# Optimization experiments

Hardware: AMD Instinct MI355X
Metric: run time of the kernel (lower is better)

The kernel has to match this reference:

```python
import jax, jax.numpy as jnp
import numpy as np

C = 256          # channels
K = 7            # kernel_size
GC = 16          # group_channels (hardcoded in module)
G = C // GC      # groups = 16
RED = 4          # reduction_ratio
PAD = (K - 1) // 2
EPS = 1e-5


def _bn(x, gamma, beta, mean, var):
    # inference-mode BatchNorm2d over channel dim (axis=1)
    inv = gamma / jnp.sqrt(var + EPS)
    return x * inv[None, :, None, None] + (beta - mean * inv)[None, :, None, None]


def setup_inputs() -> dict:
    key = jax.random.key(0)
    ks = jax.random.split(key, 8)
    cm = C // RED  # 64
    x = jax.random.normal(ks[0], (4, C, 64, 64), dtype=jnp.float32)
    w1 = jax.random.normal(ks[1], (cm, C), dtype=jnp.float32) * (1.0 / np.sqrt(C))
    bn1_gamma = jnp.abs(jax.random.normal(ks[2], (cm,), dtype=jnp.float32)) + 0.5
    bn1_beta = jax.random.normal(ks[3], (cm,), dtype=jnp.float32) * 0.1
    bn1_mean = jnp.zeros((cm,), jnp.float32)
    bn1_var = jnp.ones((cm,), jnp.float32)
    w2 = jax.random.normal(ks[4], (K * K * G, cm), dtype=jnp.float32) * (1.0 / np.sqrt(cm))
    b2 = jax.random.normal(ks[5], (K * K * G,), dtype=jnp.float32) * 0.1
    bn2_gamma = jnp.abs(jax.random.normal(ks[6], (C,), dtype=jnp.float32)) + 0.5
    bn2_beta = jax.random.normal(ks[7], (C,), dtype=jnp.float32) * 0.1
    bn2_mean = jnp.zeros((C,), jnp.float32)
    bn2_var = jnp.ones((C,), jnp.float32)
    return {"x": x, "w1": w1, "bn1_gamma": bn1_gamma, "bn1_beta": bn1_beta,
            "bn1_mean": bn1_mean, "bn1_var": bn1_var, "w2": w2, "b2": b2,
            "bn2_gamma": bn2_gamma, "bn2_beta": bn2_beta,
            "bn2_mean": bn2_mean, "bn2_var": bn2_var}


def reference(x, w1, bn1_gamma, bn1_beta, bn1_mean, bn1_var,
              w2, b2, bn2_gamma, bn2_beta, bn2_mean, bn2_var):
    b, c, h, w = x.shape
    # weight branch: 1x1 conv (no bias) -> BN -> ReLU -> 1x1 conv (bias)
    t = jnp.einsum('oc,bchw->bohw', w1, x)
    t = jax.nn.relu(_bn(t, bn1_gamma, bn1_beta, bn1_mean, bn1_var))
    wgt = jnp.einsum('oc,bchw->bohw', w2, t) + b2[None, :, None, None]
    wgt = wgt.reshape(b, G, K * K, h, w)  # per-pixel kernel per group
    # unfold x: extract KxK patches (stride 1, pad PAD), torch ordering:
    # channel slowest, kernel row, kernel col fastest
    x_pad = jnp.pad(x, ((0, 0), (0, 0), (PAD, PAD), (PAD, PAD)))
    patches = jnp.stack([x_pad[:, :, i:i + h, j:j + w]
                         for i in range(K) for j in range(K)], axis=2)  # (b,c,K2,h,w)
    patches = patches.reshape(b, G, GC, K * K, h, w)
    out = jnp.einsum('bgckhw,bgkhw->bgchw', patches, wgt).reshape(b, c, h, w)
    return jax.nn.relu(_bn(out, bn2_gamma, bn2_beta, bn2_mean, bn2_var))
```

## Files before the change

kernel.cpp:

```cpp
#include <hip/hip_runtime.h>

#define BN 4
#define C 256
#define H 64
#define W 64
#define CM 64
#define G 16
#define GC 16
#define KS 7
#define K2 49
#define PADD 3
#define EPSV 1e-5f

#define TS 16
#define HALO_R 22
#define HROWF 32
#define HSLOTP 712

#define W1T_OFF 0
#define B2P_OFF (W1T_OFF + C*CM)
#define S1_OFF  (B2P_OFF + G*64)
#define B1_OFF  (S1_OFF + CM)
#define S2_OFF  (B1_OFF + CM)
#define B2C_OFF (S2_OFF + C)
#define ZERO_OFF (B2C_OFF + C)
#define ABF_OFF (ZERO_OFF + 16)
#define TBF_OFF (ABF_OFF + 32768)

typedef __attribute__((ext_vector_type(8))) short bf16x8;
typedef __attribute__((ext_vector_type(4))) float f32x4;

__device__ __forceinline__ uint f2bf_rne(float f) {
  uint u = __float_as_uint(f);
  return (u + 0x7fffu + ((u >> 16) & 1u)) >> 16;
}

__device__ __forceinline__ void gload_lds4(const float* g, float* l) {
  __builtin_amdgcn_global_load_lds(
      (const __attribute__((address_space(1))) void*)g,
      (__attribute__((address_space(3))) void*)l, 4, 0, 0);
}

#define WAITBAR(N) do {                                            \
    asm volatile("s_waitcnt vmcnt(" #N ") lgkmcnt(0)" ::: "memory"); \
    __builtin_amdgcn_s_barrier();                                  \
    __builtin_amdgcn_sched_barrier(0);                             \
  } while (0)

#define BARRIER_ONLY() do {                                        \
    asm volatile("s_waitcnt lgkmcnt(0)" ::: "memory");             \
    __builtin_amdgcn_s_barrier();                                  \
    __builtin_amdgcn_sched_barrier(0);                             \
  } while (0)

__global__ __launch_bounds__(256) void prep_kernel(
    const float* __restrict__ w1, const float* __restrict__ w2,
    const float* __restrict__ b2,
    const float* __restrict__ g1, const float* __restrict__ be1,
    const float* __restrict__ m1, const float* __restrict__ v1,
    const float* __restrict__ g2, const float* __restrict__ be2,
    const float* __restrict__ m2, const float* __restrict__ v2,
    float* __restrict__ ws) {
  int tid = blockIdx.x * 256 + threadIdx.x;
  int nthr = gridDim.x * 256;
  for (int i = tid; i < CM * C; i += nthr) {
    int o = i / C, c = i - o * C;
    ws[W1T_OFF + c * CM + o] = w1[i];
  }
  {
    ushort* abf = (ushort*)(ws + ABF_OFF);
    for (int i = tid; i < G * 4 * 2 * 64 * 8; i += nthr) {
      int j = i & 7, lane = (i >> 3) & 63, ks = (i >> 9) & 1;
      int mt = (i >> 10) & 3, g = (i >> 12) & 15;
      int m = mt * 16 + (lane & 15);
      int o = ks * 32 + ((lane >> 4) << 3) + j;
      float v = (m < K2) ? w2[(g * K2 + m) * CM + o] : 0.f;
      abf[i] = (ushort)f2bf_rne(v);
    }
  }
  for (int i = tid; i < G * 64; i += nthr) {
    int g = i >> 6, k = i & 63;
    ws[B2P_OFF + i] = (k < K2) ? b2[g * K2 + k] : 0.f;
  }
  if (tid < CM) {
    float inv = g1[tid] * rsqrtf(v1[tid] + EPSV);
    ws[S1_OFF + tid] = inv;
    ws[B1_OFF + tid] = be1[tid] - m1[tid] * inv;
  }
  if (tid < C) {
    float inv = g2[tid] * rsqrtf(v2[tid] + EPSV);
    ws[S2_OFF + tid] = inv;
    ws[B2C_OFF + tid] = be2[tid] - m2[tid] * inv;
  }
  if (tid < 16) ws[ZERO_OFF + tid] = 0.f;
}

__global__ __launch_bounds__(256) void t_kernel(
    const float* __restrict__ x, float* __restrict__ ws) {
  __shared__ float part[4][32][64];
  int p = threadIdx.x & 63;
  int q = __builtin_amdgcn_readfirstlane(threadIdx.x >> 6);
  int y = blockIdx.x, b = blockIdx.y, oh = blockIdx.z;
  const float* __restrict__ w1T = ws + W1T_OFF + oh * 32;

  float acc[32];
#pragma unroll
  for (int o = 0; o < 32; ++o) acc[o] = 0.f;
  const float* __restrict__ xrow = x + (((size_t)b * C + q * 64) * H + y) * W;
#pragma unroll 2
  for (int cc = 0; cc < 64; ++cc) {
    float xv = xrow[(size_t)cc * H * W + p];
    const float* __restrict__ wr = w1T + (q * 64 + cc) * CM;
#pragma unroll
    for (int o = 0; o < 32; ++o) acc[o] = fmaf(wr[o], xv, acc[o]);
  }
#pragma unroll
  for (int o = 0; o < 32; ++o) part[q][o][p] = acc[o];
  __syncthreads();

  int tile = (y >> 4) * 4 + (p >> 4);
  int pix = (y & 15) * 16 + (p & 15);
  const float* __restrict__ s1 = ws + S1_OFF + oh * 32;
  const float* __restrict__ b1 = ws + B1_OFF + oh * 32;
  float fv[8];
#pragma unroll
  for (int i = 0; i < 8; ++i) {
    int o = q * 8 + i;
    float s = part[0][o][p] + part[1][o][p] + part[2][o][p] + part[3][o][p];
    fv[i] = fmaxf(fmaf(s, s1[o], b1[o]), 0.f);
  }
  uint4 pk;
  pk.x = f2bf_rne(fv[0]) | (f2bf_rne(fv[1]) << 16);
  pk.y = f2bf_rne(fv[2]) | (f2bf_rne(fv[3]) << 16);
  pk.z = f2bf_rne(fv[4]) | (f2bf_rne(fv[5]) << 16);
  pk.w = f2bf_rne(fv[6]) | (f2bf_rne(fv[7]) << 16);
  ushort* tbf = (ushort*)(ws + TBF_OFF);
  size_t idx = (((size_t)(b * 16 + tile) * 256 + pix) * 64) + oh * 32 + q * 8;
  *(uint4*)(tbf + idx) = pk;
}

__global__ __launch_bounds__(256, 3) void inv_kernel(
    const float* __restrict__ x, const float* __restrict__ ws,
    float* __restrict__ out) {
  __shared__ uint wgt_u[25][256];
  __shared__ float xh[2][4][HSLOTP];

  int tid = threadIdx.x;
  int lane = tid & 63;
  int wv = __builtin_amdgcn_readfirstlane(tid >> 6);
  int c16 = lane & 15, q = lane >> 4;
  int py = tid >> 4, chl = (tid >> 2) & 3, pq = tid & 3;
  int px0 = pq << 2;
  int tile = blockIdx.x, g = blockIdx.y, b = blockIdx.z;
  int ty = (tile >> 2) * TS, tx = (tile & 3) * TS;

  const ushort* abf = (const ushort*)(ws + ABF_OFF);
  const ushort* tbf = (const ushort*)(ws + TBF_OFF);

  float scv[4], bcv[4];
#pragma unroll
  for (int p = 0; p < 4; ++p) {
    scv[p] = ws[S2_OFF + g * GC + p * 4 + chl];
    bcv[p] = ws[B2C_OFF + g * GC + p * 4 + chl];
  }

  bf16x8 afr[4][2], bfr[4][2];
  f32x4 bias[4];
#pragma unroll
  for (int mt = 0; mt < 4; ++mt) {
#pragma unroll
    for (int ks = 0; ks < 2; ++ks)
      afr[mt][ks] = *(const bf16x8*)(abf + ((g * 8 + mt * 2 + ks) * 64 + lane) * 8);
    bias[mt] = *(const f32x4*)(ws + B2P_OFF + g * 64 + mt * 16 + q * 4);
  }
#pragma unroll
  for (int nt = 0; nt < 4; ++nt) {
    int pix = wv * 64 + nt * 16 + c16;
#pragma unroll
    for (int ks = 0; ks < 2; ++ks)
      bfr[nt][ks] = *(const bf16x8*)(
          tbf + (((size_t)(b * 16 + tile) * 256 + pix) * 64 + ks * 32 + q * 8));
  }

  uint hmask = 0;
  int hofs[11];
#pragma unroll
  for (int t2 = 0; t2 < 11; ++t2) {
    int f = t2 * 64 + lane;
    int row = f >> 5, cp = (f >> 2) & 7, sub = f & 3;
    int s8 = (row + 3 * (row >> 3)) & 7;
    int col = ((cp ^ s8) << 2) + sub;
    int gy = ty + row - PADD, gx = tx + col - PADD;
    bool v = (col < HALO_R) && ((unsigned)gy < H) && ((unsigned)gx < W);
    hmask |= (uint)v << t2;
    hofs[t2] = gy * W + gx;
  }
  const float* zsrc = ws + ZERO_OFF;
  const float* xg = x + ((size_t)b * C + g * GC) * (H * W);

#define STAGE(CH, BUF) do {                                         \
    const float* xc_ = xg + (size_t)(CH) * (H * W);                 \
    float* dst_ = &xh[BUF][(CH) & 3][0];                            \
    _Pragma("unroll")                                               \
    for (int t2 = 0; t2 < 11; ++t2) {                               \
      const float* s_ = ((hmask >> t2) & 1u) ? (xc_ + hofs[t2]) : zsrc; \
      gload_lds4(s_, dst_ + t2 * 64);                               \
    }                                                               \
  } while (0)

  STAGE(wv, 0);
  STAGE(4 + wv, 1);

#pragma unroll
  for (int nt = 0; nt < 4; ++nt) {
    f32x4 a[4];
#pragma unroll
    for (int mt = 0; mt < 4; ++mt) a[mt] = bias[mt];
#pragma unroll
    for (int ks = 0; ks < 2; ++ks)
#pragma unroll
      for (int mt = 0; mt < 4; ++mt)
        a[mt] = __builtin_amdgcn_mfma_f32_16x16x32_bf16(afr[mt][ks], bfr[nt][ks],
                                                        a[mt], 0, 0, 0);
    int pix = wv * 64 + nt * 16 + c16;
#pragma unroll
    for (int mt = 0; mt < 4; ++mt) {
      uint lo = f2bf_rne(a[mt][0]) | (f2bf_rne(a[mt][1]) << 16);
      uint hi = f2bf_rne(a[mt][2]) | (f2bf_rne(a[mt][3]) << 16);
      int j0v = mt * 8 + q * 2;
      if (j0v < 25) wgt_u[j0v][pix] = lo;
      if (j0v + 1 < 25) wgt_u[j0v + 1][pix] = hi;
    }
  }

  auto phase = [&](int bufI, int p) {
    f32x4 acc = {0.f, 0.f, 0.f, 0.f};
#pragma unroll
    for (int di = 0; di < KS; ++di) {
      const int j0 = (di * 7) >> 1;
      uint4 wq[4];
#pragma unroll
      for (int m = 0; m < 4; ++m)
        wq[m] = *(const uint4*)&wgt_u[j0 + m][py * 16 + px0];
      int row = py + di;
      int s8 = (row + 3 * (row >> 3)) & 7;
      const float* hb = &xh[bufI][chl][row * HROWF];
      f32x4 h0 = *(const f32x4*)&hb[((pq + 0) ^ s8) << 2];
      f32x4 h1 = *(const f32x4*)&hb[((pq + 1) ^ s8) << 2];
      f32x4 h2 = *(const f32x4*)&hb[((pq + 2) ^ s8) << 2];
      float rw[12] = {h0[0], h0[1], h0[2], h0[3], h1[0], h1[1],
                      h1[2], h1[3], h2[0], h2[1], h2[2], h2[3]};
#pragma unroll
      for (int dj = 0; dj < KS; ++dj) {
        const int k = di * 7 + dj, m = (k >> 1) - j0, hf = k & 1;
#pragma unroll
        for (int i = 0; i < 4; ++i) {
          uint u = (&wq[m].x)[i];
          float wf = __uint_as_float(hf ? (u & 0xffff0000u) : (u << 16));
          acc[i] = fmaf(rw[i + dj], wf, acc[i]);
        }
      }
    }
    int ch = p * 4 + chl;
    float4 o4;
    o4.x = fmaxf(fmaf(acc[0], scv[p], bcv[p]), 0.f);
    o4.y = fmaxf(fmaf(acc[1], scv[p], bcv[p]), 0.f);
    o4.z = fmaxf(fmaf(acc[2], scv[p], bcv[p]), 0.f);
    o4.w = fmaxf(fmaf(acc[3], scv[p], bcv[p]), 0.f);
    *(float4*)(out + (((size_t)b * C + g * GC + ch) * H + ty + py) * W + tx + px0) = o4;
  };

  WAITBAR(11);
  phase(0, 0);
  BARRIER_ONLY();
  STAGE(8 + wv, 0);
  WAITBAR(12);
  phase(1, 1);
  BARRIER_ONLY();
  STAGE(12 + wv, 1);
  WAITBAR(12);
  phase(0, 2);
  WAITBAR(1);
  phase(1, 3);
#undef STAGE
}

extern "C" void kernel_launch(void* const* d_in, const int* in_sizes, int n_in,
                              void* d_out, int out_size, void* d_ws, size_t ws_size,
                              hipStream_t stream) {
  const float* x   = (const float*)d_in[0];
  const float* w1  = (const float*)d_in[1];
  const float* g1  = (const float*)d_in[2];
  const float* be1 = (const float*)d_in[3];
  const float* m1  = (const float*)d_in[4];
  const float* v1  = (const float*)d_in[5];
  const float* w2  = (const float*)d_in[6];
  const float* b2  = (const float*)d_in[7];
  const float* g2  = (const float*)d_in[8];
  const float* be2 = (const float*)d_in[9];
  const float* m2  = (const float*)d_in[10];
  const float* v2  = (const float*)d_in[11];
  float* outp = (float*)d_out;
  float* ws = (float*)d_ws;

  prep_kernel<<<dim3(64), dim3(256), 0, stream>>>(w1, w2, b2, g1, be1, m1, v1,
                                                  g2, be2, m2, v2, ws);
  t_kernel<<<dim3(H, BN, 2), dim3(256), 0, stream>>>(x, ws);
  inv_kernel<<<dim3(16, G, BN), dim3(256), 0, stream>>>(x, ws, outp);
}
```

Measured before the change: 47.61 us.

## Stage x as bf16 copy and load all 16 channel halos at once

The t_kernel now also writes a bf16 copy of x to workspace, and inv_kernel stages halos for all 16 group channels from that bf16 copy in a single load phase. This replaces the double-buffered fp32 per-4-channel pipeline. Each thread then computes 4 channels per pixel quad, reusing the unpacked weights across channels. The aim is to halve halo load traffic and reuse weight decode across channels. In exchange it adds an extra global write of x, loses load/compute overlap, rounds x to bf16 (precision loss), and raises register pressure.

```diff
diff --git a/kernel.cpp b/kernel.cpp
--- a/kernel.cpp
+++ b/kernel.cpp
@@ -13,9 +13,7 @@
 #define EPSV 1e-5f
 
 #define TS 16
-#define HALO_R 22
-#define HROWF 32
-#define HSLOTP 712
+#define HSLOT_U 388
 
 #define W1T_OFF 0
 #define B2P_OFF (W1T_OFF + C*CM)
@@ -26,6 +24,7 @@
 #define ZERO_OFF (B2C_OFF + C)
 #define ABF_OFF (ZERO_OFF + 16)
 #define TBF_OFF (ABF_OFF + 32768)
+#define XBF_OFF (TBF_OFF + 524288)
 
 typedef __attribute__((ext_vector_type(8))) short bf16x8;
 typedef __attribute__((ext_vector_type(4))) float f32x4;
@@ -35,23 +34,11 @@
   return (u + 0x7fffu + ((u >> 16) & 1u)) >> 16;
 }
 
-__device__ __forceinline__ void gload_lds4(const float* g, float* l) {
+__device__ __forceinline__ void gload_lds4(const void* g, void* l) {
   __builtin_amdgcn_global_load_lds(
       (const __attribute__((address_space(1))) void*)g,
       (__attribute__((address_space(3))) void*)l, 4, 0, 0);
 }
-
-#define WAITBAR(N) do {                                            \
-    asm volatile("s_waitcnt vmcnt(" #N ") lgkmcnt(0)" ::: "memory"); \
-    __builtin_amdgcn_s_barrier();                                  \
-    __builtin_amdgcn_sched_barrier(0);                             \
-  } while (0)
-
-#define BARRIER_ONLY() do {                                        \
-    asm volatile("s_waitcnt lgkmcnt(0)" ::: "memory");             \
-    __builtin_amdgcn_s_barrier();                                  \
-    __builtin_amdgcn_sched_barrier(0);                             \
-  } while (0)
 
 __global__ __launch_bounds__(256) void prep_kernel(
     const float* __restrict__ w1, const float* __restrict__ w2,
@@ -102,6 +89,7 @@
   int q = __builtin_amdgcn_readfirstlane(threadIdx.x >> 6);
   int y = blockIdx.x, b = blockIdx.y, oh = blockIdx.z;
   const float* __restrict__ w1T = ws + W1T_OFF + oh * 32;
+  ushort* __restrict__ xbf = (ushort*)(ws + XBF_OFF);
 
   float acc[32];
 #pragma unroll
@@ -110,6 +98,8 @@
 #pragma unroll 2
   for (int cc = 0; cc < 64; ++cc) {
     float xv = xrow[(size_t)cc * H * W + p];
+    if (oh == 0)
+      xbf[(size_t)(b * C + q * 64 + cc) * (H * W) + y * W + p] = (ushort)f2bf_rne(xv);
     const float* __restrict__ wr = w1T + (q * 64 + cc) * CM;
 #pragma unroll
     for (int o = 0; o < 32; ++o) acc[o] = fmaf(wr[o], xv, acc[o]);
@@ -140,28 +130,28 @@
 }
 
 __global__ __launch_bounds__(256, 3) void inv_kernel(
-    const float* __restrict__ x, const float* __restrict__ ws,
-    float* __restrict__ out) {
+    const float* __restrict__ ws, float* __restrict__ out) {
   __shared__ uint wgt_u[25][256];
-  __shared__ float xh[2][4][HSLOTP];
+  __shared__ uint xh[G * HSLOT_U];
 
   int tid = threadIdx.x;
   int lane = tid & 63;
   int wv = __builtin_amdgcn_readfirstlane(tid >> 6);
   int c16 = lane & 15, q = lane >> 4;
-  int py = tid >> 4, chl = (tid >> 2) & 3, pq = tid & 3;
-  int px0 = pq << 2;
   int tile = blockIdx.x, g = blockIdx.y, b = blockIdx.z;
   int ty = (tile >> 2) * TS, tx = (tile & 3) * TS;
+  int py = tid >> 4, pq = (tid >> 2) & 3, chq = tid & 3;
 
   const ushort* abf = (const ushort*)(ws + ABF_OFF);
   const ushort* tbf = (const ushort*)(ws + TBF_OFF);
+  const uint* xbfu = (const uint*)(ws + XBF_OFF);
 
   float scv[4], bcv[4];
 #pragma unroll
-  for (int p = 0; p < 4; ++p) {
-    scv[p] = ws[S2_OFF + g * GC + p * 4 + chl];
-    bcv[p] = ws[B2C_OFF + g * GC + p * 4 + chl];
+  for (int ci = 0; ci < 4; ++ci) {
+    int ch = ci * 4 + chq;
+    scv[ci] = ws[S2_OFF + g * GC + ch];
+    bcv[ci] = ws[B2C_OFF + g * GC + ch];
   }
 
   bf16x8 afr[4][2], bfr[4][2];
@@ -182,34 +172,31 @@
           tbf + (((size_t)(b * 16 + tile) * 256 + pix) * 64 + ks * 32 + q * 8));
   }
 
-  uint hmask = 0;
-  int hofs[11];
-#pragma unroll
-  for (int t2 = 0; t2 < 11; ++t2) {
-    int f = t2 * 64 + lane;
-    int row = f >> 5, cp = (f >> 2) & 7, sub = f & 3;
-    int s8 = (row + 3 * (row >> 3)) & 7;
-    int col = ((cp ^ s8) << 2) + sub;
-    int gy = ty + row - PADD, gx = tx + col - PADD;
-    bool v = (col < HALO_R) && ((unsigned)gy < H) && ((unsigned)gx < W);
-    hmask |= (uint)v << t2;
-    hofs[t2] = gy * W + gx;
-  }
-  const float* zsrc = ws + ZERO_OFF;
-  const float* xg = x + ((size_t)b * C + g * GC) * (H * W);
-
-#define STAGE(CH, BUF) do {                                         \
-    const float* xc_ = xg + (size_t)(CH) * (H * W);                 \
-    float* dst_ = &xh[BUF][(CH) & 3][0];                            \
-    _Pragma("unroll")                                               \
-    for (int t2 = 0; t2 < 11; ++t2) {                               \
-      const float* s_ = ((hmask >> t2) & 1u) ? (xc_ + hofs[t2]) : zsrc; \
-      gload_lds4(s_, dst_ + t2 * 64);                               \
-    }                                                               \
-  } while (0)
-
-  STAGE(wv, 0);
-  STAGE(4 + wv, 1);
+  {
+    int hofs[6];
+    uint hmask = 0;
+#pragma unroll
+    for (int i = 0; i < 6; ++i) {
+      int s = i * 64 + lane;
+      int row = s >> 4, m = s & 15;
+      int gy = ty - 3 + row;
+      int gx0 = tx - 4 + 2 * m;
+      bool v = (m < 12) && (row < 22) && ((unsigned)gy < H) && ((unsigned)gx0 < 63);
+      hmask |= (uint)v << i;
+      hofs[i] = gy * 32 + (gx0 >> 1);
+    }
+    const uint* zsrc = (const uint*)(ws + ZERO_OFF);
+#pragma unroll
+    for (int j = 0; j < 4; ++j) {
+      int ch = wv * 4 + j;
+      const uint* src_ch = xbfu + (((size_t)(b * C + g * GC + ch) * (H * W)) >> 1);
+#pragma unroll
+      for (int i = 0; i < 6; ++i) {
+        const uint* s = ((hmask >> i) & 1u) ? (src_ch + hofs[i]) : zsrc;
+        gload_lds4(s, &xh[ch * HSLOT_U + i * 64]);
+      }
+    }
+  }
 
 #pragma unroll
   for (int nt = 0; nt < 4; ++nt) {
@@ -233,56 +220,69 @@
     }
   }
 
-  auto phase = [&](int bufI, int p) {
-    f32x4 acc = {0.f, 0.f, 0.f, 0.f};
-#pragma unroll
-    for (int di = 0; di < KS; ++di) {
-      const int j0 = (di * 7) >> 1;
-      uint4 wq[4];
-#pragma unroll
-      for (int m = 0; m < 4; ++m)
-        wq[m] = *(const uint4*)&wgt_u[j0 + m][py * 16 + px0];
-      int row = py + di;
-      int s8 = (row + 3 * (row >> 3)) & 7;
-      const float* hb = &xh[bufI][chl][row * HROWF];
-      f32x4 h0 = *(const f32x4*)&hb[((pq + 0) ^ s8) << 2];
-      f32x4 h1 = *(const f32x4*)&hb[((pq + 1) ^ s8) << 2];
-      f32x4 h2 = *(const f32x4*)&hb[((pq + 2) ^ s8) << 2];
-      float rw[12] = {h0[0], h0[1], h0[2], h0[3], h1[0], h1[1],
-                      h1[2], h1[3], h2[0], h2[1], h2[2], h2[3]};
-#pragma unroll
-      for (int dj = 0; dj < KS; ++dj) {
-        const int k = di * 7 + dj, m = (k >> 1) - j0, hf = k & 1;
-#pragma unroll
-        for (int i = 0; i < 4; ++i) {
-          uint u = (&wq[m].x)[i];
-          float wf = __uint_as_float(hf ? (u & 0xffff0000u) : (u << 16));
-          acc[i] = fmaf(rw[i + dj], wf, acc[i]);
-        }
+  asm volatile("s_waitcnt vmcnt(0) lgkmcnt(0)" ::: "memory");
+  __builtin_amdgcn_s_barrier();
+  __builtin_amdgcn_sched_barrier(0);
+
+  f32x4 acc[4];
+#pragma unroll
+  for (int ci = 0; ci < 4; ++ci) acc[ci] = (f32x4){0.f, 0.f, 0.f, 0.f};
+
+#pragma unroll
+  for (int di = 0; di < KS; ++di) {
+    const int j0 = (di * KS) >> 1;
+    uint4 wq[4];
+#pragma unroll
+    for (int m = 0; m < 4; ++m)
+      wq[m] = *(const uint4*)&wgt_u[j0 + m][py * 16 + pq * 4];
+    float wf[28];
+#pragma unroll
+    for (int dj = 0; dj < KS; ++dj) {
+      const int k = di * KS + dj;
+      const int m = (k >> 1) - j0, hf = k & 1;
+#pragma unroll
+      for (int i = 0; i < 4; ++i) {
+        uint u = (&wq[m].x)[i];
+        wf[dj * 4 + i] = __uint_as_float(hf ? (u & 0xffff0000u) : (u << 16));
       }
     }
-    int ch = p * 4 + chl;
+    int rowb = (py + di) * 16 + 2 * pq;
+#pragma unroll
+    for (int ci = 0; ci < 4; ++ci) {
+      int ch = ci * 4 + chq;
+      const uint* sl = &xh[ch * HSLOT_U + rowb];
+      uint2 r0 = *(const uint2*)(sl);
+      uint2 r1 = *(const uint2*)(sl + 2);
+      uint2 r2 = *(const uint2*)(sl + 4);
+      float hv[12];
+      hv[1] = __uint_as_float(r0.x & 0xffff0000u);
+      hv[2] = __uint_as_float(r0.y << 16);
+      hv[3] = __uint_as_float(r0.y & 0xffff0000u);
+      hv[4] = __uint_as_float(r1.x << 16);
+      hv[5] = __uint_as_float(r1.x & 0xffff0000u);
+      hv[6] = __uint_as_float(r1.y << 16);
+      hv[7] = __uint_as_float(r1.y & 0xffff0000u);
+      hv[8] = __uint_as_float(r2.x << 16);
+      hv[9] = __uint_as_float(r2.x & 0xffff0000u);
+      hv[10] = __uint_as_float(r2.y << 16);
+#pragma unroll
+      for (int dj = 0; dj < KS; ++dj)
+#pragma unroll
+        for (int i = 0; i < 4; ++i)
+          acc[ci][i] = fmaf(hv[i + dj + 1], wf[dj * 4 + i], acc[ci][i]);
+    }
+  }
+
+#pragma unroll
+  for (int ci = 0; ci < 4; ++ci) {
+    int ch = ci * 4 + chq;
     float4 o4;
-    o4.x = fmaxf(fmaf(acc[0], scv[p], bcv[p]), 0.f);
-    o4.y = fmaxf(fmaf(acc[1], scv[p], bcv[p]), 0.f);
-    o4.z = fmaxf(fmaf(acc[2], scv[p], bcv[p]), 0.f);
-    o4.w = fmaxf(fmaf(acc[3], scv[p], bcv[p]), 0.f);
-    *(float4*)(out + (((size_t)b * C + g * GC + ch) * H + ty + py) * W + tx + px0) = o4;
-  };
-
-  WAITBAR(11);
-  phase(0, 0);
-  BARRIER_ONLY();
-  STAGE(8 + wv, 0);
-  WAITBAR(12);
-  phase(1, 1);
-  BARRIER_ONLY();
-  STAGE(12 + wv, 1);
-  WAITBAR(12);
-  phase(0, 2);
-  WAITBAR(1);
-  phase(1, 3);
-#undef STAGE
+    o4.x = fmaxf(fmaf(acc[ci][0], scv[ci], bcv[ci]), 0.f);
+    o4.y = fmaxf(fmaf(acc[ci][1], scv[ci], bcv[ci]), 0.f);
+    o4.z = fmaxf(fmaf(acc[ci][2], scv[ci], bcv[ci]), 0.f);
+    o4.w = fmaxf(fmaf(acc[ci][3], scv[ci], bcv[ci]), 0.f);
+    *(float4*)(out + (((size_t)b * C + g * GC + ch) * H + ty + py) * W + tx + pq * 4) = o4;
+  }
 }
 
 extern "C" void kernel_launch(void* const* d_in, const int* in_sizes, int n_in,
@@ -306,5 +306,5 @@
   prep_kernel<<<dim3(64), dim3(256), 0, stream>>>(w1, w2, b2, g1, be1, m1, v1,
                                                   g2, be2, m2, v2, ws);
   t_kernel<<<dim3(H, BN, 2), dim3(256), 0, stream>>>(x, ws);
-  inv_kernel<<<dim3(16, G, BN), dim3(256), 0, stream>>>(x, ws, outp);
-}
+  inv_kernel<<<dim3(16, G, BN), dim3(256), 0, stream>>>(ws, outp);
+}
```

New measurement: 51.95 us. +9.1%, slower.
